# Optimization experiments

Measured on AMD Instinct MI355X. Metric: run time of the kernel, lower is better.

## Reference

```python
import jax, jax.numpy as jnp
import numpy as np

K = 15          # number of kernel points
RADIUS = 0.2    # kernel sphere radius
SIGMA = 0.05    # Gaussian influence bandwidth
C_IN = 3
C_OUT = 32
N = 65536
H = 32


def _make_kernel_points(key):
    # fixed kernel-point dispositions inside a sphere of radius RADIUS
    pts = jax.random.normal(key, (K, 3), dtype=jnp.float32)
    pts = pts / (jnp.linalg.norm(pts, axis=-1, keepdims=True) + 1e-6)
    r = jax.random.uniform(jax.random.fold_in(key, 1), (K, 1), dtype=jnp.float32) ** (1.0 / 3.0)
    return pts * r * RADIUS


def setup_inputs() -> dict:
    key = jax.random.key(0)
    k1, k2, k3, k4, k5 = jax.random.split(key, 5)
    points = jax.random.normal(k1, (N, 3), dtype=jnp.float32)
    neighbor_indices = jax.random.randint(k2, (N, H), 0, N, dtype=jnp.int64)
    kernel_points = _make_kernel_points(k3)                                   # (K, 3)
    weights = jax.random.normal(k4, (K, C_IN, C_OUT), dtype=jnp.float32) * 0.1  # (K, Cin, Cout)
    bias = jax.random.normal(k5, (C_OUT,), dtype=jnp.float32) * 0.01
    return {"points": points, "neighbor_indices": neighbor_indices,
            "kernel_points": kernel_points, "weights": weights, "bias": bias}


def reference(points, neighbor_indices, kernel_points, weights, bias):
    # feats = points (module uses point coords as input features)
    shadow_pt = jnp.full((1, 3), 1e6, dtype=points.dtype)      # shadow point far away
    s_points = jnp.concatenate([points, shadow_pt], axis=0)     # (N+1, 3)
    s_feats = jnp.concatenate([points, jnp.zeros((1, C_IN), points.dtype)], axis=0)

    nbr_pts = s_points[neighbor_indices]                        # (N, H, 3) gather
    rel = nbr_pts - points[:, None, :]                          # (N, H, 3)
    diff = rel[:, :, None, :] - kernel_points[None, None, :, :] # (N, H, K, 3)
    sq_dist = jnp.sum(diff * diff, axis=-1)                     # (N, H, K)
    influence = jnp.exp(-sq_dist / (2.0 * SIGMA * SIGMA))       # Gaussian kernel-point weighting

    nbr_feats = s_feats[neighbor_indices]                       # (N, H, Cin)
    # aggregate neighbors per kernel point, then apply per-kernel-point linear maps
    weighted = jnp.einsum('nhk,nhc->nkc', influence, nbr_feats) # (N, K, Cin)
    out = jnp.einsum('nkc,kcd->nd', weighted, weights) + bias   # (N, Cout)
    return out
```

## Files before the change

### kernel.cpp

```cpp
#include <hip/hip_runtime.h>

#define KPK 15
#define CIN 3
#define COUT 32
#define NH 32
#define LPP 4
#define HPL 8

__global__ __launch_bounds__(256) void kpconv_kernel(
    const float* __restrict__ points,
    const int*   __restrict__ nbr,
    const float* __restrict__ kpts,
    const float* __restrict__ weights,
    const float* __restrict__ bias,
    float* __restrict__ out,
    int n)
{
    __shared__ float  sW[KPK * CIN * COUT];
    __shared__ float4 sKC[KPK];
    __shared__ float  sB[COUT];

    for (int t = threadIdx.x; t < KPK * CIN * COUT; t += blockDim.x) sW[t] = weights[t];
    if (threadIdx.x < COUT) sB[threadIdx.x] = bias[threadIdx.x];
    if (threadIdx.x < KPK) {
        const float L2E = 1.44269504088896f;
        float kx = kpts[threadIdx.x * 3 + 0];
        float ky = kpts[threadIdx.x * 3 + 1];
        float kz = kpts[threadIdx.x * 3 + 2];
        float ck = kx * kx + ky * ky + kz * kz;
        sKC[threadIdx.x] = make_float4(400.0f * L2E * kx,
                                       400.0f * L2E * ky,
                                       400.0f * L2E * kz,
                                       -200.0f * L2E * ck);
    }
    __syncthreads();

    int gid = blockIdx.x * blockDim.x + threadIdx.x;
    int pt  = gid >> 2;
    int sub = gid & 3;
    if (pt >= n) return;

    float px = points[pt * 3 + 0];
    float py = points[pt * 3 + 1];
    float pz = points[pt * 3 + 2];

    const int* nb = nbr + (size_t)pt * NH + sub * HPL;
    int4 idxa = *reinterpret_cast<const int4*>(nb);
    int4 idxb = *reinterpret_cast<const int4*>(nb + 4);
    int js[HPL] = {idxa.x, idxa.y, idxa.z, idxa.w,
                   idxb.x, idxb.y, idxb.z, idxb.w};

    float acc[KPK][CIN];
    #pragma unroll
    for (int k = 0; k < KPK; ++k) { acc[k][0] = 0.f; acc[k][1] = 0.f; acc[k][2] = 0.f; }

    const float C0 = -200.0f * 1.44269504088896f;

    #pragma unroll
    for (int t = 0; t < HPL; ++t) {
        int j = js[t];
        float qx = points[j * 3 + 0];
        float qy = points[j * 3 + 1];
        float qz = points[j * 3 + 2];
        float rx = qx - px, ry = qy - py, rz = qz - pz;
        float e0 = C0 * (rx * rx + ry * ry + rz * rz);
        #pragma unroll
        for (int k = 0; k < KPK; ++k) {
            float4 kc = sKC[k];
            float e = e0 + kc.w;
            e = fmaf(rx, kc.x, e);
            e = fmaf(ry, kc.y, e);
            e = fmaf(rz, kc.z, e);
            float infl = exp2f(e);
            acc[k][0] = fmaf(infl, qx, acc[k][0]);
            acc[k][1] = fmaf(infl, qy, acc[k][1]);
            acc[k][2] = fmaf(infl, qz, acc[k][2]);
        }
    }

    #pragma unroll
    for (int m = 1; m < LPP; m <<= 1) {
        #pragma unroll
        for (int k = 0; k < KPK; ++k) {
            acc[k][0] += __shfl_xor(acc[k][0], m, 64);
            acc[k][1] += __shfl_xor(acc[k][1], m, 64);
            acc[k][2] += __shfl_xor(acc[k][2], m, 64);
        }
    }

    int d0 = sub * 8;
    float4 o0 = *reinterpret_cast<const float4*>(sB + d0);
    float4 o1 = *reinterpret_cast<const float4*>(sB + d0 + 4);
    #pragma unroll
    for (int k = 0; k < KPK; ++k) {
        #pragma unroll
        for (int c = 0; c < CIN; ++c) {
            float a = acc[k][c];
            const float* w = sW + (k * CIN + c) * COUT + d0;
            float4 w0 = *reinterpret_cast<const float4*>(w);
            float4 w1 = *reinterpret_cast<const float4*>(w + 4);
            o0.x = fmaf(a, w0.x, o0.x);
            o0.y = fmaf(a, w0.y, o0.y);
            o0.z = fmaf(a, w0.z, o0.z);
            o0.w = fmaf(a, w0.w, o0.w);
            o1.x = fmaf(a, w1.x, o1.x);
            o1.y = fmaf(a, w1.y, o1.y);
            o1.z = fmaf(a, w1.z, o1.z);
            o1.w = fmaf(a, w1.w, o1.w);
        }
    }

    float* op = out + (size_t)pt * COUT + d0;
    *reinterpret_cast<float4*>(op)     = o0;
    *reinterpret_cast<float4*>(op + 4) = o1;
}

extern "C" void kernel_launch(void* const* d_in, const int* in_sizes, int n_in,
                              void* d_out, int out_size, void* d_ws, size_t ws_size,
                              hipStream_t stream) {
    const float* points  = (const float*)d_in[0];
    const int*   nbr     = (const int*)d_in[1];
    const float* kpts    = (const float*)d_in[2];
    const float* weights = (const float*)d_in[3];
    const float* bias    = (const float*)d_in[4];
    float* out = (float*)d_out;

    int n = in_sizes[0] / 3;
    int total = n * LPP;
    int threads = 256;
    int blocks = (total + threads - 1) / threads;
    kpconv_kernel<<<blocks, threads, 0, stream>>>(points, nbr, kpts, weights, bias, out, n);
}
```

Baseline: 84.42 us.

## Pack points to float4, halve lanes per point, prefetch neighbor gathers

Adds a pre-pass that packs the xyz points into padded float4 in the workspace, so each neighbor gather becomes a single 16-byte load instead of three scalar loads. The split changes from 4 lanes per point to 2, with each lane handling 16 neighbors and 16 output channels. All neighbor coordinates are loaded up front to expose memory-level parallelism. exp2f is replaced by the raw hardware exp2 builtin. The price is an extra kernel launch, workspace traffic, higher register pressure from the larger q array and accumulators, and half as many threads.

```diff
diff --git a/kernel.cpp b/kernel.cpp
--- a/kernel.cpp
+++ b/kernel.cpp
@@ -4,11 +4,18 @@
 #define CIN 3
 #define COUT 32
 #define NH 32
-#define LPP 4
-#define HPL 8
+#define LPP 2
+#define HPL 16
+
+__global__ __launch_bounds__(256) void pack_points_kernel(
+    const float* __restrict__ pts, float4* __restrict__ p4, int n)
+{
+    int i = blockIdx.x * blockDim.x + threadIdx.x;
+    if (i < n) p4[i] = make_float4(pts[3*i], pts[3*i+1], pts[3*i+2], 0.f);
+}
 
 __global__ __launch_bounds__(256) void kpconv_kernel(
-    const float* __restrict__ points,
+    const float4* __restrict__ p4,
     const int*   __restrict__ nbr,
     const float* __restrict__ kpts,
     const float* __restrict__ weights,
@@ -36,19 +43,23 @@
     __syncthreads();
 
     int gid = blockIdx.x * blockDim.x + threadIdx.x;
-    int pt  = gid >> 2;
-    int sub = gid & 3;
+    int pt  = gid >> 1;
+    int sub = gid & 1;
     if (pt >= n) return;
 
-    float px = points[pt * 3 + 0];
-    float py = points[pt * 3 + 1];
-    float pz = points[pt * 3 + 2];
+    float4 p = p4[pt];
 
     const int* nb = nbr + (size_t)pt * NH + sub * HPL;
-    int4 idxa = *reinterpret_cast<const int4*>(nb);
-    int4 idxb = *reinterpret_cast<const int4*>(nb + 4);
-    int js[HPL] = {idxa.x, idxa.y, idxa.z, idxa.w,
-                   idxb.x, idxb.y, idxb.z, idxb.w};
+    int js[HPL];
+    #pragma unroll
+    for (int t = 0; t < HPL / 4; ++t) {
+        int4 v = *reinterpret_cast<const int4*>(nb + 4 * t);
+        js[4*t+0] = v.x; js[4*t+1] = v.y; js[4*t+2] = v.z; js[4*t+3] = v.w;
+    }
+
+    float4 q[HPL];
+    #pragma unroll
+    for (int t = 0; t < HPL; ++t) q[t] = p4[js[t]];
 
     float acc[KPK][CIN];
     #pragma unroll
@@ -58,11 +69,8 @@
 
     #pragma unroll
     for (int t = 0; t < HPL; ++t) {
-        int j = js[t];
-        float qx = points[j * 3 + 0];
-        float qy = points[j * 3 + 1];
-        float qz = points[j * 3 + 2];
-        float rx = qx - px, ry = qy - py, rz = qz - pz;
+        float qx = q[t].x, qy = q[t].y, qz = q[t].z;
+        float rx = qx - p.x, ry = qy - p.y, rz = qz - p.z;
         float e0 = C0 * (rx * rx + ry * ry + rz * rz);
         #pragma unroll
         for (int k = 0; k < KPK; ++k) {
@@ -71,7 +79,7 @@
             e = fmaf(rx, kc.x, e);
             e = fmaf(ry, kc.y, e);
             e = fmaf(rz, kc.z, e);
-            float infl = exp2f(e);
+            float infl = __builtin_amdgcn_exp2f(e);
             acc[k][0] = fmaf(infl, qx, acc[k][0]);
             acc[k][1] = fmaf(infl, qy, acc[k][1]);
             acc[k][2] = fmaf(infl, qz, acc[k][2]);
@@ -79,18 +87,17 @@
     }
 
     #pragma unroll
-    for (int m = 1; m < LPP; m <<= 1) {
-        #pragma unroll
-        for (int k = 0; k < KPK; ++k) {
-            acc[k][0] += __shfl_xor(acc[k][0], m, 64);
-            acc[k][1] += __shfl_xor(acc[k][1], m, 64);
-            acc[k][2] += __shfl_xor(acc[k][2], m, 64);
-        }
+    for (int k = 0; k < KPK; ++k) {
+        acc[k][0] += __shfl_xor(acc[k][0], 1, 64);
+        acc[k][1] += __shfl_xor(acc[k][1], 1, 64);
+        acc[k][2] += __shfl_xor(acc[k][2], 1, 64);
     }
 
-    int d0 = sub * 8;
+    int d0 = sub * 16;
     float4 o0 = *reinterpret_cast<const float4*>(sB + d0);
     float4 o1 = *reinterpret_cast<const float4*>(sB + d0 + 4);
+    float4 o2 = *reinterpret_cast<const float4*>(sB + d0 + 8);
+    float4 o3 = *reinterpret_cast<const float4*>(sB + d0 + 12);
     #pragma unroll
     for (int k = 0; k < KPK; ++k) {
         #pragma unroll
@@ -99,20 +106,24 @@
             const float* w = sW + (k * CIN + c) * COUT + d0;
             float4 w0 = *reinterpret_cast<const float4*>(w);
             float4 w1 = *reinterpret_cast<const float4*>(w + 4);
-            o0.x = fmaf(a, w0.x, o0.x);
-            o0.y = fmaf(a, w0.y, o0.y);
-            o0.z = fmaf(a, w0.z, o0.z);
-            o0.w = fmaf(a, w0.w, o0.w);
-            o1.x = fmaf(a, w1.x, o1.x);
-            o1.y = fmaf(a, w1.y, o1.y);
-            o1.z = fmaf(a, w1.z, o1.z);
-            o1.w = fmaf(a, w1.w, o1.w);
+            float4 w2 = *reinterpret_cast<const float4*>(w + 8);
+            float4 w3 = *reinterpret_cast<const float4*>(w + 12);
+            o0.x = fmaf(a, w0.x, o0.x); o0.y = fmaf(a, w0.y, o0.y);
+            o0.z = fmaf(a, w0.z, o0.z); o0.w = fmaf(a, w0.w, o0.w);
+            o1.x = fmaf(a, w1.x, o1.x); o1.y = fmaf(a, w1.y, o1.y);
+            o1.z = fmaf(a, w1.z, o1.z); o1.w = fmaf(a, w1.w, o1.w);
+            o2.x = fmaf(a, w2.x, o2.x); o2.y = fmaf(a, w2.y, o2.y);
+            o2.z = fmaf(a, w2.z, o2.z); o2.w = fmaf(a, w2.w, o2.w);
+            o3.x = fmaf(a, w3.x, o3.x); o3.y = fmaf(a, w3.y, o3.y);
+            o3.z = fmaf(a, w3.z, o3.z); o3.w = fmaf(a, w3.w, o3.w);
         }
     }
 
     float* op = out + (size_t)pt * COUT + d0;
-    *reinterpret_cast<float4*>(op)     = o0;
-    *reinterpret_cast<float4*>(op + 4) = o1;
+    *reinterpret_cast<float4*>(op)      = o0;
+    *reinterpret_cast<float4*>(op + 4)  = o1;
+    *reinterpret_cast<float4*>(op + 8)  = o2;
+    *reinterpret_cast<float4*>(op + 12) = o3;
 }
 
 extern "C" void kernel_launch(void* const* d_in, const int* in_sizes, int n_in,
@@ -126,8 +137,12 @@
     float* out = (float*)d_out;
 
     int n = in_sizes[0] / 3;
+    float4* p4 = (float4*)d_ws;
+
+    int threads = 256;
+    pack_points_kernel<<<(n + threads - 1) / threads, threads, 0, stream>>>(points, p4, n);
+
     int total = n * LPP;
-    int threads = 256;
     int blocks = (total + threads - 1) / threads;
-    kpconv_kernel<<<blocks, threads, 0, stream>>>(points, nbr, kpts, weights, bias, out, n);
+    kpconv_kernel<<<blocks, threads, 0, stream>>>(p4, nbr, kpts, weights, bias, out, n);
 }
```

Result: slower. 87.74 us (+3.9%).
